# Performance work log

Hardware: AMD Instinct MI355X
Metric: run time of the kernel (lower is better)

Reference implementation:

```python
import jax, jax.numpy as jnp
import numpy as np


def setup_inputs() -> dict:
    key = jax.random.key(0)
    k = jax.random.split(key, 7)
    B, IN, OUT = 128, 1024, 1024
    return {
        "x": jax.random.normal(k[0], (B, IN), dtype=jnp.float32),
        "eps": jax.random.normal(k[1], (B, IN, OUT), dtype=jnp.float32),
        "eps_bias": jax.random.normal(k[2], (B, OUT), dtype=jnp.float32),
        "mu": jax.random.normal(k[3], (IN, OUT), dtype=jnp.float32),
        "ro": jax.random.normal(k[4], (IN, OUT), dtype=jnp.float32),
        "mu_bias": jax.random.normal(k[5], (1, OUT), dtype=jnp.float32),
        "ro_bias": jax.random.normal(k[6], (1, OUT), dtype=jnp.float32),
    }


def reference(x, eps, eps_bias, mu, ro, mu_bias, ro_bias):
    # softplus: log(1 + exp(ro)) as written in the original module
    sigma = jnp.log1p(jnp.exp(ro))            # [in, out]
    sigma_bias = jnp.log1p(jnp.exp(ro_bias))  # [1, out]
    weights = eps * sigma + mu                # [B, in, out] per-sample weights
    bias = eps_bias * sigma_bias + mu_bias    # [B, out]
    # (x.unsqueeze(1) @ weights).squeeze() -> per-sample matvec
    return jnp.einsum("bi,bio->bo", x, weights) + bias
```

## Files before the change

kernel.cpp:

```cpp
#include <hip/hip_runtime.h>
#include <math.h>

#define BB 128
#define IN 1024
#define OUTD 1024
#define ISPLIT 8
#define ICHUNK (IN / ISPLIT)

typedef float f4v __attribute__((ext_vector_type(4)));

__device__ __forceinline__ float softplus(float r) {
    return fmaxf(r, 0.0f) + log1pf(expf(-fabsf(r)));
}

__global__ __launch_bounds__(256) void prep_sigma(const float* __restrict__ ro,
                                                  float* __restrict__ sigma) {
    int idx = blockIdx.x * 256 + threadIdx.x;
    float4 r = ((const float4*)ro)[idx];
    float4 s;
    s.x = softplus(r.x);
    s.y = softplus(r.y);
    s.z = softplus(r.z);
    s.w = softplus(r.w);
    ((float4*)sigma)[idx] = s;
}

__global__ __launch_bounds__(256, 2) void bayes_main(
    const float* __restrict__ x, const float* __restrict__ eps,
    const float* __restrict__ mu, const float* __restrict__ sigma,
    float* __restrict__ partial) {
    __shared__ float xs[8][ICHUNK];
    const int tid = threadIdx.x;
    const int b0 = blockIdx.x * 8;
    const int o0 = blockIdx.y * 256;
    const int i0 = blockIdx.z * ICHUNK;

    for (int t = tid; t < 8 * ICHUNK; t += 256) {
        int bb = t / ICHUNK, ii = t % ICHUNK;
        xs[bb][ii] = x[(size_t)(b0 + bb) * IN + i0 + ii];
    }
    __syncthreads();

    const int oq = tid & 63;
    const int bsub = tid >> 6;
    const int o = o0 + oq * 4;

    const float4* sp = (const float4*)(sigma + (size_t)i0 * OUTD + o);
    const float4* mp = (const float4*)(mu + (size_t)i0 * OUTD + o);
    const f4v* e0p = (const f4v*)(eps + ((size_t)(b0 + bsub) * IN + i0) * OUTD + o);
    const f4v* e1p =
        (const f4v*)(eps + ((size_t)(b0 + 4 + bsub) * IN + i0) * OUTD + o);

    float4 acc0 = {0.f, 0.f, 0.f, 0.f};
    float4 acc1 = {0.f, 0.f, 0.f, 0.f};

#pragma unroll 8
    for (int ii = 0; ii < ICHUNK; ++ii) {
        float4 s = sp[(size_t)ii * (OUTD / 4)];
        float4 m = mp[(size_t)ii * (OUTD / 4)];
        f4v e0 = __builtin_nontemporal_load(e0p + (size_t)ii * (OUTD / 4));
        f4v e1 = __builtin_nontemporal_load(e1p + (size_t)ii * (OUTD / 4));
        float x0 = xs[bsub][ii];
        float x1 = xs[bsub + 4][ii];
        acc0.x = fmaf(x0, fmaf(e0.x, s.x, m.x), acc0.x);
        acc0.y = fmaf(x0, fmaf(e0.y, s.y, m.y), acc0.y);
        acc0.z = fmaf(x0, fmaf(e0.z, s.z, m.z), acc0.z);
        acc0.w = fmaf(x0, fmaf(e0.w, s.w, m.w), acc0.w);
        acc1.x = fmaf(x1, fmaf(e1.x, s.x, m.x), acc1.x);
        acc1.y = fmaf(x1, fmaf(e1.y, s.y, m.y), acc1.y);
        acc1.z = fmaf(x1, fmaf(e1.z, s.z, m.z), acc1.z);
        acc1.w = fmaf(x1, fmaf(e1.w, s.w, m.w), acc1.w);
    }

    const int is = blockIdx.z;
    float* pp0 = partial + ((size_t)is * BB + (b0 + bsub)) * OUTD + o;
    *(float4*)pp0 = acc0;
    float* pp1 = partial + ((size_t)is * BB + (b0 + 4 + bsub)) * OUTD + o;
    *(float4*)pp1 = acc1;
}

__global__ __launch_bounds__(256) void finalize(
    const float* __restrict__ partial, const float* __restrict__ eps_bias,
    const float* __restrict__ mu_bias, const float* __restrict__ ro_bias,
    float* __restrict__ out) {
    int idx = blockIdx.x * 256 + threadIdx.x;
    int p = idx * 4;
    int o = p & (OUTD - 1);

    float4 acc = {0.f, 0.f, 0.f, 0.f};
#pragma unroll
    for (int is = 0; is < ISPLIT; ++is) {
        float4 a = *(const float4*)(partial + (size_t)is * BB * OUTD + p);
        acc.x += a.x;
        acc.y += a.y;
        acc.z += a.z;
        acc.w += a.w;
    }
    float4 eb = *(const float4*)(eps_bias + p);
    float4 rb = *(const float4*)(ro_bias + o);
    float4 mb = *(const float4*)(mu_bias + o);

    float4 r;
    r.x = acc.x + eb.x * softplus(rb.x) + mb.x;
    r.y = acc.y + eb.y * softplus(rb.y) + mb.y;
    r.z = acc.z + eb.z * softplus(rb.z) + mb.z;
    r.w = acc.w + eb.w * softplus(rb.w) + mb.w;
    ((float4*)out)[idx] = r;
}

extern "C" void kernel_launch(void* const* d_in, const int* in_sizes, int n_in,
                              void* d_out, int out_size, void* d_ws, size_t ws_size,
                              hipStream_t stream) {
    const float* x = (const float*)d_in[0];
    const float* eps = (const float*)d_in[1];
    const float* eps_bias = (const float*)d_in[2];
    const float* mu = (const float*)d_in[3];
    const float* ro = (const float*)d_in[4];
    const float* mu_bias = (const float*)d_in[5];
    const float* ro_bias = (const float*)d_in[6];
    float* out = (float*)d_out;

    float* sigma = (float*)d_ws;
    float* partial = sigma + (size_t)IN * OUTD;

    prep_sigma<<<(IN * OUTD / 4) / 256, 256, 0, stream>>>(ro, sigma);

    dim3 grid(BB / 8, OUTD / 256, ISPLIT);
    bayes_main<<<grid, 256, 0, stream>>>(x, eps, mu, sigma, partial);

    finalize<<<(BB * OUTD / 4) / 256, 256, 0, stream>>>(partial, eps_bias, mu_bias,
                                                        ro_bias, out);
}
```

Measured before the change: 111.1 us.

## Remap bayes_main to one batch row per block over the full output width

Each block now handles a single batch sample, one input chunk and all 1024 outputs, with each thread covering 4 outputs, in place of 8 samples by 256 outputs. The change removes the reuse of sigma and mu loads across 8 samples in a block, relying on cache for reuse across blocks. In return each thread keeps fewer live registers, the occupancy hint rises to 4, and each warp reads longer contiguous eps rows. The eps stream dominates traffic, so the expected gain comes from better latency hiding and access pattern, at the cost of more sigma/mu traffic through L2.

```diff
diff --git a/kernel.cpp b/kernel.cpp
--- a/kernel.cpp
+++ b/kernel.cpp
@@ -25,58 +25,40 @@
     ((float4*)sigma)[idx] = s;
 }
 
-__global__ __launch_bounds__(256, 2) void bayes_main(
+__global__ __launch_bounds__(256, 4) void bayes_main(
     const float* __restrict__ x, const float* __restrict__ eps,
     const float* __restrict__ mu, const float* __restrict__ sigma,
     float* __restrict__ partial) {
-    __shared__ float xs[8][ICHUNK];
+    __shared__ float xs[ICHUNK];
     const int tid = threadIdx.x;
-    const int b0 = blockIdx.x * 8;
-    const int o0 = blockIdx.y * 256;
-    const int i0 = blockIdx.z * ICHUNK;
+    const int b = blockIdx.x;
+    const int is = blockIdx.y;
+    const int i0 = is * ICHUNK;
 
-    for (int t = tid; t < 8 * ICHUNK; t += 256) {
-        int bb = t / ICHUNK, ii = t % ICHUNK;
-        xs[bb][ii] = x[(size_t)(b0 + bb) * IN + i0 + ii];
-    }
+    if (tid < ICHUNK) xs[tid] = x[(size_t)b * IN + i0 + tid];
     __syncthreads();
 
-    const int oq = tid & 63;
-    const int bsub = tid >> 6;
-    const int o = o0 + oq * 4;
-
+    const int o = tid * 4;
     const float4* sp = (const float4*)(sigma + (size_t)i0 * OUTD + o);
     const float4* mp = (const float4*)(mu + (size_t)i0 * OUTD + o);
-    const f4v* e0p = (const f4v*)(eps + ((size_t)(b0 + bsub) * IN + i0) * OUTD + o);
-    const f4v* e1p =
-        (const f4v*)(eps + ((size_t)(b0 + 4 + bsub) * IN + i0) * OUTD + o);
+    const f4v* ep = (const f4v*)(eps + ((size_t)b * IN + i0) * OUTD + o);
 
-    float4 acc0 = {0.f, 0.f, 0.f, 0.f};
-    float4 acc1 = {0.f, 0.f, 0.f, 0.f};
+    float4 acc = {0.f, 0.f, 0.f, 0.f};
 
-#pragma unroll 8
+#pragma unroll 4
     for (int ii = 0; ii < ICHUNK; ++ii) {
         float4 s = sp[(size_t)ii * (OUTD / 4)];
         float4 m = mp[(size_t)ii * (OUTD / 4)];
-        f4v e0 = __builtin_nontemporal_load(e0p + (size_t)ii * (OUTD / 4));
-        f4v e1 = __builtin_nontemporal_load(e1p + (size_t)ii * (OUTD / 4));
-        float x0 = xs[bsub][ii];
-        float x1 = xs[bsub + 4][ii];
-        acc0.x = fmaf(x0, fmaf(e0.x, s.x, m.x), acc0.x);
-        acc0.y = fmaf(x0, fmaf(e0.y, s.y, m.y), acc0.y);
-        acc0.z = fmaf(x0, fmaf(e0.z, s.z, m.z), acc0.z);
-        acc0.w = fmaf(x0, fmaf(e0.w, s.w, m.w), acc0.w);
-        acc1.x = fmaf(x1, fmaf(e1.x, s.x, m.x), acc1.x);
-        acc1.y = fmaf(x1, fmaf(e1.y, s.y, m.y), acc1.y);
-        acc1.z = fmaf(x1, fmaf(e1.z, s.z, m.z), acc1.z);
-        acc1.w = fmaf(x1, fmaf(e1.w, s.w, m.w), acc1.w);
+        f4v e = __builtin_nontemporal_load(ep + (size_t)ii * (OUTD / 4));
+        float xv = xs[ii];
+        acc.x = fmaf(xv, fmaf(e.x, s.x, m.x), acc.x);
+        acc.y = fmaf(xv, fmaf(e.y, s.y, m.y), acc.y);
+        acc.z = fmaf(xv, fmaf(e.z, s.z, m.z), acc.z);
+        acc.w = fmaf(xv, fmaf(e.w, s.w, m.w), acc.w);
     }
 
-    const int is = blockIdx.z;
-    float* pp0 = partial + ((size_t)is * BB + (b0 + bsub)) * OUTD + o;
-    *(float4*)pp0 = acc0;
-    float* pp1 = partial + ((size_t)is * BB + (b0 + 4 + bsub)) * OUTD + o;
-    *(float4*)pp1 = acc1;
+    float* pp = partial + ((size_t)is * BB + b) * OUTD + o;
+    *(float4*)pp = acc;
 }
 
 __global__ __launch_bounds__(256) void finalize(
@@ -125,7 +107,7 @@
 
     prep_sigma<<<(IN * OUTD / 4) / 256, 256, 0, stream>>>(ro, sigma);
 
-    dim3 grid(BB / 8, OUTD / 256, ISPLIT);
+    dim3 grid(BB, ISPLIT);
     bayes_main<<<grid, 256, 0, stream>>>(x, eps, mu, sigma, partial);
 
     finalize<<<(BB * OUTD / 4) / 256, 256, 0, stream>>>(partial, eps_bias, mu_bias,
```

After: 147.1 us. +32.4%, slower.
